# Kernel optimization log

Hardware: AMD Instinct MI355X
Metric: run time of the kernel (lower is better)

The kernel has to match this reference:

```python
import jax, jax.numpy as jnp
import numpy as np

BS, NF, C, H, W = 2, 16, 32, 128, 128
NUM_MASKS, NUM_CLASSES = 8, 3


def setup_inputs() -> dict:
    key = jax.random.key(0)
    k1, k2, k3 = jax.random.split(key, 3)
    dec_fts = jax.random.normal(k1, (BS, NF, C, H, W), dtype=jnp.float32)
    seg_w = jax.random.normal(k2, (NUM_MASKS, C), dtype=jnp.float32) * 0.1
    seg_b = jnp.zeros((NUM_MASKS,), dtype=jnp.float32)
    logits_w = jax.random.normal(k3, (NUM_CLASSES, C), dtype=jnp.float32) * 0.1
    logits_b = jnp.zeros((NUM_CLASSES,), dtype=jnp.float32)
    return {"dec_fts": dec_fts, "seg_w": seg_w, "seg_b": seg_b,
            "logits_w": logits_w, "logits_b": logits_b}


def reference(dec_fts, seg_w, seg_b, logits_w, logits_b):
    bs, n_frames, c, h, w = dec_fts.shape
    mid = n_frames // 2
    # segmentation head: 1x1 conv on the middle frame -> (bs, num_masks, h, w)
    masks = jnp.einsum('bchw,mc->bmhw', dec_fts[:, mid], seg_w) + seg_b[None, :, None, None]
    # mask-weighted spatial pooling: avoids the (bs,nf,m,c,h,w) intermediate
    pooled = jnp.einsum('bfchw,bmhw->bmfc', dec_fts, masks)  # (bs, m, nf, c)
    # head_3d == 'avg': mean over frames -> (bs, m, c)
    pooled = pooled.mean(axis=2)
    # per-mask linear head, flatten to (bs, m*num_classes)
    logits = jnp.einsum('bmc,kc->bmk', pooled, logits_w) + logits_b
    logits = logits.reshape(bs, -1)
    return (logits, masks)
```

## Files before the change

kernel.cpp:

```cpp
#include <hip/hip_runtime.h>

#define BS 2
#define NF 16
#define CH 32
#define HW 16384
#define NM 8
#define NK 3
#define MID 8

#define S 64
#define BPB (HW / S)
#define NBLK (BS * BPB)

__global__ __launch_bounds__(512, 4) void fused_kernel(
    const float* __restrict__ dec, const float* __restrict__ seg_w,
    const float* __restrict__ seg_b, float* __restrict__ masks_out,
    float* __restrict__ part) {
  __shared__ float mid[CH][S];
  __shared__ float msk[NM][S];
  __shared__ float pbuf[NM * CH];

  int t = threadIdx.x;
  int bid = blockIdx.x;
  int b = bid >> 8;
  int chunk = bid & 255;
  int cs = chunk * S;

  int s = t & 15;
  int c = t >> 4;

  const float* base = dec + ((size_t)(b * NF) * CH + c) * HW + cs + s * 4;
  float4 x[NF];
  x[MID] = *(const float4*)(base + (size_t)MID * CH * HW);
#pragma unroll
  for (int f = 0; f < NF; ++f)
    if (f != MID) x[f] = *(const float4*)(base + (size_t)f * CH * HW);

  *(float4*)&mid[c][s * 4] = x[MID];
  __syncthreads();

  {
    int m = t >> 6, px = t & 63;
    float v = seg_b[m];
#pragma unroll
    for (int cc = 0; cc < CH; ++cc) v += mid[cc][px] * seg_w[m * CH + cc];
    msk[m][px] = v;
    masks_out[(size_t)b * NM * HW + (size_t)m * HW + cs + px] = v;
  }
  __syncthreads();

  float4 w[NM];
#pragma unroll
  for (int m = 0; m < NM; ++m) w[m] = *(const float4*)&msk[m][s * 4];

  float acc[NM];
#pragma unroll
  for (int m = 0; m < NM; ++m) acc[m] = 0.f;
#pragma unroll
  for (int f = 0; f < NF; ++f)
#pragma unroll
    for (int m = 0; m < NM; ++m)
      acc[m] += x[f].x * w[m].x + x[f].y * w[m].y + x[f].z * w[m].z +
                x[f].w * w[m].w;

#pragma unroll
  for (int off = 8; off >= 1; off >>= 1)
#pragma unroll
    for (int m = 0; m < NM; ++m) acc[m] += __shfl_down(acc[m], off, 16);

  if (s == 0)
#pragma unroll
    for (int m = 0; m < NM; ++m) pbuf[m * CH + c] = acc[m];
  __syncthreads();
  if (t < NM * CH) part[(size_t)bid * (NM * CH) + t] = pbuf[t];
}

__global__ __launch_bounds__(1024) void reduce_head_kernel(
    const float* __restrict__ part, const float* __restrict__ lw,
    const float* __restrict__ lb, float* __restrict__ out) {
  __shared__ float red[32][CH];
  __shared__ float pooled[CH];

  int t = threadIdx.x;
  int b = blockIdx.x >> 3;
  int m = blockIdx.x & 7;

  int c = t & 31, j = t >> 5;
  float sum = 0.f;
  const float* p = part + (size_t)b * BPB * (NM * CH) + m * CH + c;
  for (int i = j; i < BPB; i += 32)
    sum += p[(size_t)i * (NM * CH)];
  red[j][c] = sum;
  __syncthreads();

  if (t < CH) {
    float v = 0.f;
#pragma unroll
    for (int jj = 0; jj < 32; ++jj) v += red[jj][t];
    pooled[t] = v * (1.0f / NF);
  }
  __syncthreads();

  if (t < NK) {
    float dot = 0.f;
#pragma unroll
    for (int cc = 0; cc < CH; ++cc) dot += pooled[cc] * lw[t * CH + cc];
    out[b * (NM * NK) + m * NK + t] = dot + lb[t];
  }
}

extern "C" void kernel_launch(void* const* d_in, const int* in_sizes, int n_in,
                              void* d_out, int out_size, void* d_ws,
                              size_t ws_size, hipStream_t stream) {
  const float* dec = (const float*)d_in[0];
  const float* seg_w = (const float*)d_in[1];
  const float* seg_b = (const float*)d_in[2];
  const float* lw = (const float*)d_in[3];
  const float* lb = (const float*)d_in[4];

  float* out = (float*)d_out;
  float* logits_out = out;
  float* masks_out = out + BS * NM * NK;
  float* part = (float*)d_ws;

  fused_kernel<<<NBLK, 512, 0, stream>>>(dec, seg_w, seg_b, masks_out, part);
  reduce_head_kernel<<<BS * NM, 1024, 0, stream>>>(part, lw, lb, logits_out);
}
```

Baseline: 102.7 us.

## Fuse reduction head into main kernel via atomic completion counter

Removes the separate reduce/head kernel launch by having the first 16 blocks spin on a global atomic counter until all blocks have written partials, then perform the final reduction and linear head. A memset of the counter is added before the launch. This trades a kernel launch gap for a memset node plus spin-waiting blocks. It relies on all 512 blocks being co-resident or on the low-index blocks being scheduled first, which avoids deadlock only in practice.

Result: slower. 120.0 us (+16.8%).

```diff
diff --git a/kernel.cpp b/kernel.cpp
--- a/kernel.cpp
+++ b/kernel.cpp
@@ -11,14 +11,19 @@
 #define S 64
 #define BPB (HW / S)
 #define NBLK (BS * BPB)
+#define PROW (NM * CH)
 
 __global__ __launch_bounds__(512, 4) void fused_kernel(
     const float* __restrict__ dec, const float* __restrict__ seg_w,
-    const float* __restrict__ seg_b, float* __restrict__ masks_out,
-    float* __restrict__ part) {
+    const float* __restrict__ seg_b, const float* __restrict__ lw,
+    const float* __restrict__ lb, float* __restrict__ masks_out,
+    float* __restrict__ logits_out, float* __restrict__ part,
+    unsigned int* __restrict__ counter) {
   __shared__ float mid[CH][S];
   __shared__ float msk[NM][S];
-  __shared__ float pbuf[NM * CH];
+  __shared__ float pbuf[PROW];
+  __shared__ float red[16][CH];
+  __shared__ float pooled[CH];
 
   int t = threadIdx.x;
   int bid = blockIdx.x;
@@ -72,40 +77,47 @@
 #pragma unroll
     for (int m = 0; m < NM; ++m) pbuf[m * CH + c] = acc[m];
   __syncthreads();
-  if (t < NM * CH) part[(size_t)bid * (NM * CH) + t] = pbuf[t];
-}
+  if (t < PROW) part[(size_t)bid * PROW + t] = pbuf[t];
 
-__global__ __launch_bounds__(1024) void reduce_head_kernel(
-    const float* __restrict__ part, const float* __restrict__ lw,
-    const float* __restrict__ lb, float* __restrict__ out) {
-  __shared__ float red[32][CH];
-  __shared__ float pooled[CH];
+  __syncthreads();
+  if (t == 0) {
+    __threadfence();
+    __hip_atomic_fetch_add(counter, 1u, __ATOMIC_RELEASE,
+                           __HIP_MEMORY_SCOPE_AGENT);
+  }
 
-  int t = threadIdx.x;
-  int b = blockIdx.x >> 3;
-  int m = blockIdx.x & 7;
+  if (bid < BS * NM) {
+    if (t == 0) {
+      while (__hip_atomic_load(counter, __ATOMIC_ACQUIRE,
+                               __HIP_MEMORY_SCOPE_AGENT) < NBLK)
+        __builtin_amdgcn_s_sleep(16);
+      __threadfence();
+    }
+    __syncthreads();
 
-  int c = t & 31, j = t >> 5;
-  float sum = 0.f;
-  const float* p = part + (size_t)b * BPB * (NM * CH) + m * CH + c;
-  for (int i = j; i < BPB; i += 32)
-    sum += p[(size_t)i * (NM * CH)];
-  red[j][c] = sum;
-  __syncthreads();
+    int rb = bid >> 3, rm = bid & 7;
+    int rc = t & 31, j = t >> 5;
+    float sum = 0.f;
+    const float* p = part + (size_t)rb * BPB * PROW + rm * CH + rc;
+    for (int i = j; i < BPB; i += 16)
+      sum += p[(size_t)i * PROW];
+    red[j][rc] = sum;
+    __syncthreads();
 
-  if (t < CH) {
-    float v = 0.f;
+    if (t < CH) {
+      float v = 0.f;
 #pragma unroll
-    for (int jj = 0; jj < 32; ++jj) v += red[jj][t];
-    pooled[t] = v * (1.0f / NF);
-  }
-  __syncthreads();
+      for (int jj = 0; jj < 16; ++jj) v += red[jj][t];
+      pooled[t] = v * (1.0f / NF);
+    }
+    __syncthreads();
 
-  if (t < NK) {
-    float dot = 0.f;
+    if (t < NK) {
+      float dot = 0.f;
 #pragma unroll
-    for (int cc = 0; cc < CH; ++cc) dot += pooled[cc] * lw[t * CH + cc];
-    out[b * (NM * NK) + m * NK + t] = dot + lb[t];
+      for (int cc = 0; cc < CH; ++cc) dot += pooled[cc] * lw[t * CH + cc];
+      logits_out[rb * (NM * NK) + rm * NK + t] = dot + lb[t];
+    }
   }
 }
 
@@ -122,7 +134,9 @@
   float* logits_out = out;
   float* masks_out = out + BS * NM * NK;
   float* part = (float*)d_ws;
+  unsigned int* counter = (unsigned int*)((char*)d_ws + NBLK * PROW * 4);
 
-  fused_kernel<<<NBLK, 512, 0, stream>>>(dec, seg_w, seg_b, masks_out, part);
-  reduce_head_kernel<<<BS * NM, 1024, 0, stream>>>(part, lw, lb, logits_out);
+  hipMemsetAsync(counter, 0, sizeof(unsigned int), stream);
+  fused_kernel<<<NBLK, 512, 0, stream>>>(dec, seg_w, seg_b, lw, lb, masks_out,
+                                         logits_out, part, counter);
 }
```
